# Kernel optimization log

Hardware: AMD Instinct MI355X
Metric: run time of the kernel (lower is better)

## Reference

```python
import jax, jax.numpy as jnp
import numpy as np

B, N, C, H = 8, 2048, 384, 6
D = C // H  # head dim = 64
SCALE = D ** -0.5


def setup_inputs() -> dict:
    key = jax.random.key(0)
    k1, k2, k3, k4 = jax.random.split(key, 4)
    x = jax.random.normal(k1, (B, N, C), dtype=jnp.float32)
    prompt = jnp.zeros((1,), dtype=jnp.float32)  # unused by forward
    mask = jax.random.uniform(k2, (B, N, N), dtype=jnp.float32)
    qkv_w = jax.random.normal(k3, (3 * C, C), dtype=jnp.float32) * (C ** -0.5)
    proj_w = jax.random.normal(k4, (C, C), dtype=jnp.float32) * (C ** -0.5)
    proj_b = jnp.zeros((C,), dtype=jnp.float32)
    return {"x": x, "prompt": prompt, "mask": mask,
            "qkv_w": qkv_w, "proj_w": proj_w, "proj_b": proj_b}


def reference(x, prompt, mask, qkv_w, proj_w, proj_b):
    b, n, c = x.shape
    # qkv: Linear(dim, 3*dim, bias=False) -> (B,N,3,H,D) -> (3,B,H,N,D)
    qkv = (x @ qkv_w.T).reshape(b, n, 3, H, D).transpose(2, 0, 3, 1, 4)
    q, k, v = qkv[0], qkv[1], qkv[2]
    # attn scores with additive mask (mask * -1e5), softmax over keys
    attn = jnp.einsum('bhqd,bhkd->bhqk', q, k) * SCALE
    attn = attn + (mask * -100000.0)[:, None, :, :]
    attn = jax.nn.softmax(attn, axis=-1)
    out = jnp.einsum('bhqk,bhkd->bhqd', attn, v)  # (B,H,N,D)
    out = out.transpose(0, 2, 1, 3).reshape(b, n, c)
    return out @ proj_w.T + proj_b
```

## Files before the change

kernel.cpp:

```cpp
#include <hip/hip_runtime.h>
#include <stdint.h>
#include <math.h>

#define BB 8
#define SEQ 2048
#define CDIM 384
#define NH 6
#define HD 64
#define QKVN 1152

typedef __attribute__((ext_vector_type(8))) __bf16 bf16x8;
typedef __attribute__((ext_vector_type(4))) __bf16 bf16x4;
typedef __attribute__((ext_vector_type(4))) float f32x4;
typedef __attribute__((ext_vector_type(4))) unsigned short ushort4v;

__device__ __forceinline__ unsigned short f2bf(float f) {
  unsigned int u = __float_as_uint(f);
  u += 0x7fffu + ((u >> 16) & 1u);
  return (unsigned short)(u >> 16);
}

__global__ void k_convert(const float* __restrict__ src, unsigned short* __restrict__ dst, int n4) {
  int i = blockIdx.x * blockDim.x + threadIdx.x;
  if (i >= n4) return;
  float4 f = reinterpret_cast<const float4*>(src)[i];
  ushort4v u;
  u.x = f2bf(f.x); u.y = f2bf(f.y); u.z = f2bf(f.z); u.w = f2bf(f.w);
  reinterpret_cast<ushort4v*>(dst)[i] = u;
}

__device__ __forceinline__ void gload_lds16(const unsigned short* g, unsigned short* l) {
  __builtin_amdgcn_global_load_lds((const __attribute__((address_space(1))) void*)g,
                                   (__attribute__((address_space(3))) void*)l, 16, 0, 0);
}

template<int OUT_F32>
__global__ __launch_bounds__(256, 2) void k_gemm_bt(
    const unsigned short* __restrict__ A, const unsigned short* __restrict__ Bm,
    unsigned short* __restrict__ Cb, float* __restrict__ Cf,
    const float* __restrict__ bias, int M, int Nc, int K)
{
  __shared__ unsigned short lA[128 * 32];
  __shared__ unsigned short lB[128 * 32];
  const int t = threadIdx.x;
  const int w = t >> 6, l = t & 63;
  const int wr = w >> 1, wc = w & 1;
  const int row0 = blockIdx.x * 128, col0 = blockIdx.y * 128;
  const f32x4 vzero = {0.f, 0.f, 0.f, 0.f};
  f32x4 acc[4][4];
#pragma unroll
  for (int m = 0; m < 4; ++m)
#pragma unroll
    for (int n = 0; n < 4; ++n) acc[m][n] = vzero;

  const int srow = w * 16 + (l >> 2);
  const int scol = (l & 3) * 8;
  const int lr = l & 15, kc = (l >> 4) * 8;

  for (int k0 = 0; k0 < K; k0 += 32) {
#pragma unroll
    for (int r = 0; r < 2; ++r) {
      gload_lds16(A + (size_t)(row0 + r * 64 + srow) * K + k0 + scol,
                  &lA[(r * 64 + srow) * 32 + scol]);
      gload_lds16(Bm + (size_t)(col0 + r * 64 + srow) * K + k0 + scol,
                  &lB[(r * 64 + srow) * 32 + scol]);
    }
    __syncthreads();
    bf16x8 af[4], bfr[4];
#pragma unroll
    for (int m = 0; m < 4; ++m)
      af[m] = *(const bf16x8*)&lA[(wr * 64 + m * 16 + lr) * 32 + kc];
#pragma unroll
    for (int n = 0; n < 4; ++n)
      bfr[n] = *(const bf16x8*)&lB[(wc * 64 + n * 16 + lr) * 32 + kc];
#pragma unroll
    for (int m = 0; m < 4; ++m)
#pragma unroll
      for (int n = 0; n < 4; ++n)
        acc[m][n] = __builtin_amdgcn_mfma_f32_16x16x32_bf16(af[m], bfr[n], acc[m][n], 0, 0, 0);
    __syncthreads();
  }

#pragma unroll
  for (int m = 0; m < 4; ++m) {
    const int row = row0 + wr * 64 + m * 16 + (l >> 4) * 4;
#pragma unroll
    for (int n = 0; n < 4; ++n) {
      const int col = col0 + wc * 64 + n * 16 + (l & 15);
      if (OUT_F32) {
        const float bv = bias[col];
#pragma unroll
        for (int j = 0; j < 4; ++j)
          Cf[(size_t)(row + j) * Nc + col] = acc[m][n][j] + bv;
      } else {
#pragma unroll
        for (int j = 0; j < 4; ++j)
          Cb[(size_t)(row + j) * Nc + col] = f2bf(acc[m][n][j]);
      }
    }
  }
}

__global__ void k_vtrans(const unsigned short* __restrict__ qkv, unsigned short* __restrict__ vt)
{
  __shared__ unsigned short tile[64][76];
  const int bh = blockIdx.x;
  const int b = bh / NH, h = bh - b * NH;
  const int n0 = blockIdx.y * 64;
  const int t = threadIdx.x;
  const int rr0 = t >> 4;
  const int c4 = (t & 15) * 4;
  const unsigned short* src = qkv + (size_t)(b * SEQ + n0) * QKVN + 2 * CDIM + h * HD;
#pragma unroll
  for (int rr = 0; rr < 4; ++rr) {
    int n = rr * 16 + rr0;
    ushort4v v = *(const ushort4v*)(src + (size_t)n * QKVN + c4);
    *(ushort4v*)&tile[n][c4] = v;
  }
  __syncthreads();
  unsigned short* dst = vt + (size_t)bh * HD * SEQ + n0;
#pragma unroll
  for (int rr = 0; rr < 4; ++rr) {
    int d = rr * 16 + rr0;
    ushort4v v;
    v.x = tile[c4 + 0][d];
    v.y = tile[c4 + 1][d];
    v.z = tile[c4 + 2][d];
    v.w = tile[c4 + 3][d];
    *(ushort4v*)(dst + (size_t)d * SEQ + c4) = v;
  }
}

__global__ __launch_bounds__(256, 3) void k_attn(
    const unsigned short* __restrict__ qkv, const float* __restrict__ mask,
    const unsigned short* __restrict__ vt, unsigned short* __restrict__ aout)
{
  const int bid = blockIdx.x;
  const int b = bid & 7;
  const int g2 = bid >> 3;
  const int h = g2 % NH;
  const int nt = g2 / NH;
  const int t = threadIdx.x;
  const int w = t >> 6, l = t & 63;
  const int gk = l >> 4, c = l & 15;
  const int q0 = nt * 128 + w * 16;

  __shared__ unsigned short lK[2][4096];
  __shared__ unsigned short lV[2][4096];

  const unsigned short* qb0 = qkv + (size_t)(b * SEQ + q0) * QKVN + h * HD;
  const unsigned short* qb1 = qb0 + (size_t)64 * QKVN;
  const unsigned short* kb = qkv + (size_t)(b * SEQ) * QKVN + CDIM + h * HD;
  const unsigned short* vb = vt + (size_t)(b * NH + h) * HD * SEQ;
  const float* mrow0 = mask + ((size_t)b * SEQ + q0 + c) * SEQ + 4 * gk;
  const float* mrow1 = mrow0 + (size_t)64 * SEQ;

  const int trow = t >> 3, tg = t & 7;
  const int glog = tg ^ (trow & 7);
  const size_t kSrc = (size_t)trow * QKVN + glog * 8;
  const size_t vSrc = (size_t)trow * SEQ + glog * 8;
  const int tid8 = t * 8;

  const int fr0 = c * 64 + ((gk) ^ (c & 7)) * 8;
  const int fr1 = c * 64 + ((4 + gk) ^ (c & 7)) * 8;
  const int cx2 = 2 * (c & 7);
  const int vg0 = c * 64 + ((gk) ^ cx2) * 4;
  const int vg1 = c * 64 + ((4 + gk) ^ cx2) * 4;
  const int vg2 = c * 64 + ((8 + gk) ^ cx2) * 4;
  const int vg3 = c * 64 + ((12 + gk) ^ cx2) * 4;

  bf16x8 qf00 = *(const bf16x8*)(qb0 + (size_t)c * QKVN + gk * 8);
  bf16x8 qf01 = *(const bf16x8*)(qb0 + (size_t)c * QKVN + 32 + gk * 8);
  bf16x8 qf10 = *(const bf16x8*)(qb1 + (size_t)c * QKVN + gk * 8);
  bf16x8 qf11 = *(const bf16x8*)(qb1 + (size_t)c * QKVN + 32 + gk * 8);
#pragma unroll
  for (int i = 0; i < 8; ++i) {
    qf00[i] = (__bf16)((float)qf00[i] * 0.18033688f);
    qf01[i] = (__bf16)((float)qf01[i] * 0.18033688f);
    qf10[i] = (__bf16)((float)qf10[i] * 0.18033688f);
    qf11[i] = (__bf16)((float)qf11[i] * 0.18033688f);
  }

  const __bf16 one = (__bf16)1.0f;
  const bf16x8 vones = {one, one, one, one, one, one, one, one};
  const f32x4 vzero = {0.f, 0.f, 0.f, 0.f};
  f32x4 acco0[4], acco1[4];
  f32x4 asum0 = vzero, asum1 = vzero;
  float mreg0 = -INFINITY, mreg1 = -INFINITY;
#pragma unroll
  for (int dt = 0; dt < 4; ++dt) { acco0[dt] = vzero; acco1[dt] = vzero; }

#pragma unroll
  for (int j = 0; j < 2; ++j) {
    gload_lds16(kb + (size_t)j * 32 * QKVN + kSrc, &lK[0][j * 2048 + tid8]);
    gload_lds16(vb + (size_t)j * 32 * SEQ + vSrc, &lV[0][j * 2048 + tid8]);
  }
  int buf = 0;

  for (int kt = 0; kt < SEQ; kt += 64) {
    const bool haveNext = (kt + 64 < SEQ);
    __syncthreads();
    if (haveNext) {
#pragma unroll
      for (int j = 0; j < 2; ++j) {
        gload_lds16(kb + (size_t)(kt + 64 + j * 32) * QKVN + kSrc, &lK[buf ^ 1][j * 2048 + tid8]);
        gload_lds16(vb + (kt + 64) + (size_t)j * 32 * SEQ + vSrc, &lV[buf ^ 1][j * 2048 + tid8]);
      }
    }

    float4 mk0[4], mk1[4];
#pragma unroll
    for (int j = 0; j < 4; ++j) {
      mk0[j] = *(const float4*)(mrow0 + kt + 16 * j);
      mk1[j] = *(const float4*)(mrow1 + kt + 16 * j);
    }

    f32x4 s0[4], s1[4];
    __builtin_amdgcn_s_setprio(1);
#pragma unroll
    for (int j = 0; j < 4; ++j) {
      bf16x8 kfa = *(const bf16x8*)&lK[buf][j * 1024 + fr0];
      bf16x8 kfb = *(const bf16x8*)&lK[buf][j * 1024 + fr1];
      s0[j] = __builtin_amdgcn_mfma_f32_16x16x32_bf16(kfa, qf00, vzero, 0, 0, 0);
      s0[j] = __builtin_amdgcn_mfma_f32_16x16x32_bf16(kfb, qf01, s0[j], 0, 0, 0);
      s1[j] = __builtin_amdgcn_mfma_f32_16x16x32_bf16(kfa, qf10, vzero, 0, 0, 0);
      s1[j] = __builtin_amdgcn_mfma_f32_16x16x32_bf16(kfb, qf11, s1[j], 0, 0, 0);
    }
    __builtin_amdgcn_s_setprio(0);

#pragma unroll
    for (int j = 0; j < 4; ++j) {
      const float* m0 = (const float*)&mk0[j];
      const float* m1 = (const float*)&mk1[j];
#pragma unroll
      for (int r = 0; r < 4; ++r) {
        s0[j][r] = fmaf(m0[r], -144269.50f, s0[j][r]);
        s1[j][r] = fmaf(m1[r], -144269.50f, s1[j][r]);
      }
    }

    float a0 = fmaxf(fmaxf(s0[0][0], s0[0][1]), s0[0][2]);
    float b0 = fmaxf(fmaxf(s0[0][3], s0[1][0]), s0[1][1]);
    float d0 = fmaxf(fmaxf(s0[1][2], s0[1][3]), s0[2][0]);
    float e0 = fmaxf(fmaxf(s0[2][1], s0[2][2]), s0[2][3]);
    float f0 = fmaxf(fmaxf(s0[3][0], s0[3][1]), s0[3][2]);
    float tm0 = fmaxf(fmaxf(fmaxf(a0, b0), d0), fmaxf(fmaxf(e0, f0), s0[3][3]));
    float a1 = fmaxf(fmaxf(s1[0][0], s1[0][1]), s1[0][2]);
    float b1 = fmaxf(fmaxf(s1[0][3], s1[1][0]), s1[1][1]);
    float d1 = fmaxf(fmaxf(s1[1][2], s1[1][3]), s1[2][0]);
    float e1 = fmaxf(fmaxf(s1[2][1], s1[2][2]), s1[2][3]);
    float f1 = fmaxf(fmaxf(s1[3][0], s1[3][1]), s1[3][2]);
    float tm1 = fmaxf(fmaxf(fmaxf(a1, b1), d1), fmaxf(fmaxf(e1, f1), s1[3][3]));
    tm0 = fmaxf(tm0, __shfl_xor(tm0, 16));
    tm1 = fmaxf(tm1, __shfl_xor(tm1, 16));
    tm0 = fmaxf(tm0, __shfl_xor(tm0, 32));
    tm1 = fmaxf(tm1, __shfl_xor(tm1, 32));

    if (__any(tm0 > mreg0 + 8.f)) {
      const float mn = fmaxf(mreg0, tm0);
      const float al = __builtin_amdgcn_exp2f(mreg0 - mn);
      mreg0 = mn;
      float alr[4];
#pragma unroll
      for (int r = 0; r < 4; ++r) alr[r] = __shfl(al, 20 * gk + r);
#pragma unroll
      for (int r = 0; r < 4; ++r) asum0[r] *= alr[r];
#pragma unroll
      for (int dt = 0; dt < 4; ++dt)
#pragma unroll
        for (int r = 0; r < 4; ++r) acco0[dt][r] *= alr[r];
    }
    if (__any(tm1 > mreg1 + 8.f)) {
      const float mn = fmaxf(mreg1, tm1);
      const float al = __builtin_amdgcn_exp2f(mreg1 - mn);
      mreg1 = mn;
      float alr[4];
#pragma unroll
      for (int r = 0; r < 4; ++r) alr[r] = __shfl(al, 20 * gk + r);
#pragma unroll
      for (int r = 0; r < 4; ++r) asum1[r] *= alr[r];
#pragma unroll
      for (int dt = 0; dt < 4; ++dt)
#pragma unroll
        for (int r = 0; r < 4; ++r) acco1[dt][r] *= alr[r];
    }

#pragma unroll
    for (int j = 0; j < 4; ++j)
#pragma unroll
      for (int r = 0; r < 4; ++r) {
        s0[j][r] = __builtin_amdgcn_exp2f(s0[j][r] - mreg0);
        s1[j][r] = __builtin_amdgcn_exp2f(s1[j][r] - mreg1);
      }

    union { unsigned int u[8]; bf16x8 v[2]; } pu0, pu1;
#pragma unroll
    for (int j = 0; j < 4; ++j) {
      asm("v_cvt_pk_bf16_f32 %0, %1, %2" : "=v"(pu0.u[2 * j]) : "v"(s0[j][0]), "v"(s0[j][1]));
      asm("v_cvt_pk_bf16_f32 %0, %1, %2" : "=v"(pu0.u[2 * j + 1]) : "v"(s0[j][2]), "v"(s0[j][3]));
      asm("v_cvt_pk_bf16_f32 %0, %1, %2" : "=v"(pu1.u[2 * j]) : "v"(s1[j][0]), "v"(s1[j][1]));
      asm("v_cvt_pk_bf16_f32 %0, %1, %2" : "=v"(pu1.u[2 * j + 1]) : "v"(s1[j][2]), "v"(s1[j][3]));
    }

    __builtin_amdgcn_s_setprio(1);
    asum0 = __builtin_amdgcn_mfma_f32_16x16x32_bf16(pu0.v[0], vones, asum0, 0, 0, 0);
    asum0 = __builtin_amdgcn_mfma_f32_16x16x32_bf16(pu0.v[1], vones, asum0, 0, 0, 0);
    asum1 = __builtin_amdgcn_mfma_f32_16x16x32_bf16(pu1.v[0], vones, asum1, 0, 0, 0);
    asum1 = __builtin_amdgcn_mfma_f32_16x16x32_bf16(pu1.v[1], vones, asum1, 0, 0, 0);
#pragma unroll
    for (int dt = 0; dt < 4; ++dt) {
      const unsigned short* vrow = &lV[buf][dt * 1024];
      bf16x4 a0v = *(const bf16x4*)(vrow + vg0);
      bf16x4 a1v = *(const bf16x4*)(vrow + vg1);
      bf16x4 a2v = *(const bf16x4*)(vrow + vg2);
      bf16x4 a3v = *(const bf16x4*)(vrow + vg3);
      bf16x8 vf0 = __builtin_shufflevector(a0v, a1v, 0, 1, 2, 3, 4, 5, 6, 7);
      bf16x8 vf1 = __builtin_shufflevector(a2v, a3v, 0, 1, 2, 3, 4, 5, 6, 7);
      acco0[dt] = __builtin_amdgcn_mfma_f32_16x16x32_bf16(pu0.v[0], vf0, acco0[dt], 0, 0, 0);
      acco0[dt] = __builtin_amdgcn_mfma_f32_16x16x32_bf16(pu0.v[1], vf1, acco0[dt], 0, 0, 0);
      acco1[dt] = __builtin_amdgcn_mfma_f32_16x16x32_bf16(pu1.v[0], vf0, acco1[dt], 0, 0, 0);
      acco1[dt] = __builtin_amdgcn_mfma_f32_16x16x32_bf16(pu1.v[1], vf1, acco1[dt], 0, 0, 0);
    }
    __builtin_amdgcn_s_setprio(0);
    buf ^= 1;
  }

  float inv0[4], inv1[4];
#pragma unroll
  for (int r = 0; r < 4; ++r) {
    inv0[r] = 1.0f / asum0[r];
    inv1[r] = 1.0f / asum1[r];
  }
  unsigned short* ob0 = aout + (size_t)(b * SEQ + q0) * CDIM + h * HD;
  unsigned short* ob1 = ob0 + (size_t)64 * CDIM;
#pragma unroll
  for (int r = 0; r < 4; ++r)
#pragma unroll
    for (int dt = 0; dt < 4; ++dt) {
      ob0[(size_t)(4 * gk + r) * CDIM + dt * 16 + c] = f2bf(acco0[dt][r] * inv0[r]);
      ob1[(size_t)(4 * gk + r) * CDIM + dt * 16 + c] = f2bf(acco1[dt][r] * inv1[r]);
    }
}

extern "C" void kernel_launch(void* const* d_in, const int* in_sizes, int n_in,
                              void* d_out, int out_size, void* d_ws, size_t ws_size,
                              hipStream_t stream) {
  (void)in_sizes; (void)n_in; (void)out_size; (void)ws_size;
  const float* x      = (const float*)d_in[0];
  const float* mask   = (const float*)d_in[2];
  const float* qkv_w  = (const float*)d_in[3];
  const float* proj_w = (const float*)d_in[4];
  const float* proj_b = (const float*)d_in[5];
  float* out = (float*)d_out;
  char* ws = (char*)d_ws;

  unsigned short* xb    = (unsigned short*)(ws + 0);
  unsigned short* wqb   = (unsigned short*)(ws + 12582912);
  unsigned short* wpb   = (unsigned short*)(ws + 13467648);
  unsigned short* qkvb  = (unsigned short*)(ws + 13762560);
  unsigned short* vtb   = (unsigned short*)(ws + 51511296);
  unsigned short* aoutb = (unsigned short*)(ws + 64094208);

  k_convert<<<6144, 256, 0, stream>>>(x, xb, 1572864);
  k_convert<<<432, 256, 0, stream>>>(qkv_w, wqb, 110592);
  k_convert<<<144, 256, 0, stream>>>(proj_w, wpb, 36864);
  k_gemm_bt<0><<<dim3(128, 9), 256, 0, stream>>>(xb, wqb, qkvb, nullptr, nullptr, 16384, 1152, 384);
  k_vtrans<<<dim3(48, 32), 256, 0, stream>>>(qkvb, vtb);
  k_attn<<<768, 256, 0, stream>>>(qkvb, mask, vtb, aoutb);
  k_gemm_bt<1><<<dim3(128, 3), 256, 0, stream>>>(aoutb, wpb, nullptr, out, proj_b, 16384, 384, 384);
}
```

Measured before the change: 174.4 us.

## Software-pipeline PV MFMA of previous tile with QK of current tile

Restructures the attention loop so the P·V and row-sum MFMAs for the previous key tile run right after the QK MFMAs of the current tile, before that tile's softmax. The V tile ring becomes a triple buffer so the previous tile's V stays resident while the next one is loaded. A final PV step after the loop handles the last tile. The aim is to overlap the matrix-core work with the exp/max VALU work, at the cost of more LDS and more registers, since the packed P values stay live across iterations.

```diff
diff --git a/kernel.cpp b/kernel.cpp
--- a/kernel.cpp
+++ b/kernel.cpp
@@ -146,7 +146,7 @@
   const int q0 = nt * 128 + w * 16;
 
   __shared__ unsigned short lK[2][4096];
-  __shared__ unsigned short lV[2][4096];
+  __shared__ unsigned short lV[3][4096];
 
   const unsigned short* qb0 = qkv + (size_t)(b * SEQ + q0) * QKVN + h * HD;
   const unsigned short* qb1 = qb0 + (size_t)64 * QKVN;
@@ -190,12 +190,17 @@
 #pragma unroll
   for (int dt = 0; dt < 4; ++dt) { acco0[dt] = vzero; acco1[dt] = vzero; }
 
+  union PU { unsigned int u[8]; bf16x8 v[2]; };
+  PU pu0 = {}, pu1 = {};
+
 #pragma unroll
   for (int j = 0; j < 2; ++j) {
     gload_lds16(kb + (size_t)j * 32 * QKVN + kSrc, &lK[0][j * 2048 + tid8]);
     gload_lds16(vb + (size_t)j * 32 * SEQ + vSrc, &lV[0][j * 2048 + tid8]);
   }
-  int buf = 0;
+  int bufK = 0;
+  int vst = 1;
+  int vpv = 2;
 
   for (int kt = 0; kt < SEQ; kt += 64) {
     const bool haveNext = (kt + 64 < SEQ);
@@ -203,8 +208,8 @@
     if (haveNext) {
 #pragma unroll
       for (int j = 0; j < 2; ++j) {
-        gload_lds16(kb + (size_t)(kt + 64 + j * 32) * QKVN + kSrc, &lK[buf ^ 1][j * 2048 + tid8]);
-        gload_lds16(vb + (kt + 64) + (size_t)j * 32 * SEQ + vSrc, &lV[buf ^ 1][j * 2048 + tid8]);
+        gload_lds16(kb + (size_t)(kt + 64 + j * 32) * QKVN + kSrc, &lK[bufK ^ 1][j * 2048 + tid8]);
+        gload_lds16(vb + (kt + 64) + (size_t)j * 32 * SEQ + vSrc, &lV[vst][j * 2048 + tid8]);
       }
     }
 
@@ -219,12 +224,32 @@
     __builtin_amdgcn_s_setprio(1);
 #pragma unroll
     for (int j = 0; j < 4; ++j) {
-      bf16x8 kfa = *(const bf16x8*)&lK[buf][j * 1024 + fr0];
-      bf16x8 kfb = *(const bf16x8*)&lK[buf][j * 1024 + fr1];
+      bf16x8 kfa = *(const bf16x8*)&lK[bufK][j * 1024 + fr0];
+      bf16x8 kfb = *(const bf16x8*)&lK[bufK][j * 1024 + fr1];
       s0[j] = __builtin_amdgcn_mfma_f32_16x16x32_bf16(kfa, qf00, vzero, 0, 0, 0);
       s0[j] = __builtin_amdgcn_mfma_f32_16x16x32_bf16(kfb, qf01, s0[j], 0, 0, 0);
       s1[j] = __builtin_amdgcn_mfma_f32_16x16x32_bf16(kfa, qf10, vzero, 0, 0, 0);
       s1[j] = __builtin_amdgcn_mfma_f32_16x16x32_bf16(kfb, qf11, s1[j], 0, 0, 0);
+    }
+    if (kt > 0) {
+      asum0 = __builtin_amdgcn_mfma_f32_16x16x32_bf16(pu0.v[0], vones, asum0, 0, 0, 0);
+      asum0 = __builtin_amdgcn_mfma_f32_16x16x32_bf16(pu0.v[1], vones, asum0, 0, 0, 0);
+      asum1 = __builtin_amdgcn_mfma_f32_16x16x32_bf16(pu1.v[0], vones, asum1, 0, 0, 0);
+      asum1 = __builtin_amdgcn_mfma_f32_16x16x32_bf16(pu1.v[1], vones, asum1, 0, 0, 0);
+#pragma unroll
+      for (int dt = 0; dt < 4; ++dt) {
+        const unsigned short* vrow = &lV[vpv][dt * 1024];
+        bf16x4 a0v = *(const bf16x4*)(vrow + vg0);
+        bf16x4 a1v = *(const bf16x4*)(vrow + vg1);
+        bf16x4 a2v = *(const bf16x4*)(vrow + vg2);
+        bf16x4 a3v = *(const bf16x4*)(vrow + vg3);
+        bf16x8 vf0 = __builtin_shufflevector(a0v, a1v, 0, 1, 2, 3, 4, 5, 6, 7);
+        bf16x8 vf1 = __builtin_shufflevector(a2v, a3v, 0, 1, 2, 3, 4, 5, 6, 7);
+        acco0[dt] = __builtin_amdgcn_mfma_f32_16x16x32_bf16(pu0.v[0], vf0, acco0[dt], 0, 0, 0);
+        acco0[dt] = __builtin_amdgcn_mfma_f32_16x16x32_bf16(pu0.v[1], vf1, acco0[dt], 0, 0, 0);
+        acco1[dt] = __builtin_amdgcn_mfma_f32_16x16x32_bf16(pu1.v[0], vf0, acco1[dt], 0, 0, 0);
+        acco1[dt] = __builtin_amdgcn_mfma_f32_16x16x32_bf16(pu1.v[1], vf1, acco1[dt], 0, 0, 0);
+      }
     }
     __builtin_amdgcn_s_setprio(0);
 
@@ -292,8 +317,6 @@
         s0[j][r] = __builtin_amdgcn_exp2f(s0[j][r] - mreg0);
         s1[j][r] = __builtin_amdgcn_exp2f(s1[j][r] - mreg1);
       }
-
-    union { unsigned int u[8]; bf16x8 v[2]; } pu0, pu1;
 #pragma unroll
     for (int j = 0; j < 4; ++j) {
       asm("v_cvt_pk_bf16_f32 %0, %1, %2" : "=v"(pu0.u[2 * j]) : "v"(s0[j][0]), "v"(s0[j][1]));
@@ -302,27 +325,28 @@
       asm("v_cvt_pk_bf16_f32 %0, %1, %2" : "=v"(pu1.u[2 * j + 1]) : "v"(s1[j][2]), "v"(s1[j][3]));
     }
 
-    __builtin_amdgcn_s_setprio(1);
-    asum0 = __builtin_amdgcn_mfma_f32_16x16x32_bf16(pu0.v[0], vones, asum0, 0, 0, 0);
-    asum0 = __builtin_amdgcn_mfma_f32_16x16x32_bf16(pu0.v[1], vones, asum0, 0, 0, 0);
-    asum1 = __builtin_amdgcn_mfma_f32_16x16x32_bf16(pu1.v[0], vones, asum1, 0, 0, 0);
-    asum1 = __builtin_amdgcn_mfma_f32_16x16x32_bf16(pu1.v[1], vones, asum1, 0, 0, 0);
-#pragma unroll
-    for (int dt = 0; dt < 4; ++dt) {
-      const unsigned short* vrow = &lV[buf][dt * 1024];
-      bf16x4 a0v = *(const bf16x4*)(vrow + vg0);
-      bf16x4 a1v = *(const bf16x4*)(vrow + vg1);
-      bf16x4 a2v = *(const bf16x4*)(vrow + vg2);
-      bf16x4 a3v = *(const bf16x4*)(vrow + vg3);
-      bf16x8 vf0 = __builtin_shufflevector(a0v, a1v, 0, 1, 2, 3, 4, 5, 6, 7);
-      bf16x8 vf1 = __builtin_shufflevector(a2v, a3v, 0, 1, 2, 3, 4, 5, 6, 7);
-      acco0[dt] = __builtin_amdgcn_mfma_f32_16x16x32_bf16(pu0.v[0], vf0, acco0[dt], 0, 0, 0);
-      acco0[dt] = __builtin_amdgcn_mfma_f32_16x16x32_bf16(pu0.v[1], vf1, acco0[dt], 0, 0, 0);
-      acco1[dt] = __builtin_amdgcn_mfma_f32_16x16x32_bf16(pu1.v[0], vf0, acco1[dt], 0, 0, 0);
-      acco1[dt] = __builtin_amdgcn_mfma_f32_16x16x32_bf16(pu1.v[1], vf1, acco1[dt], 0, 0, 0);
-    }
-    __builtin_amdgcn_s_setprio(0);
-    buf ^= 1;
+    bufK ^= 1;
+    vst = (vst == 2) ? 0 : vst + 1;
+    vpv = (vpv == 2) ? 0 : vpv + 1;
+  }
+
+  asum0 = __builtin_amdgcn_mfma_f32_16x16x32_bf16(pu0.v[0], vones, asum0, 0, 0, 0);
+  asum0 = __builtin_amdgcn_mfma_f32_16x16x32_bf16(pu0.v[1], vones, asum0, 0, 0, 0);
+  asum1 = __builtin_amdgcn_mfma_f32_16x16x32_bf16(pu1.v[0], vones, asum1, 0, 0, 0);
+  asum1 = __builtin_amdgcn_mfma_f32_16x16x32_bf16(pu1.v[1], vones, asum1, 0, 0, 0);
+#pragma unroll
+  for (int dt = 0; dt < 4; ++dt) {
+    const unsigned short* vrow = &lV[vpv][dt * 1024];
+    bf16x4 a0v = *(const bf16x4*)(vrow + vg0);
+    bf16x4 a1v = *(const bf16x4*)(vrow + vg1);
+    bf16x4 a2v = *(const bf16x4*)(vrow + vg2);
+    bf16x4 a3v = *(const bf16x4*)(vrow + vg3);
+    bf16x8 vf0 = __builtin_shufflevector(a0v, a1v, 0, 1, 2, 3, 4, 5, 6, 7);
+    bf16x8 vf1 = __builtin_shufflevector(a2v, a3v, 0, 1, 2, 3, 4, 5, 6, 7);
+    acco0[dt] = __builtin_amdgcn_mfma_f32_16x16x32_bf16(pu0.v[0], vf0, acco0[dt], 0, 0, 0);
+    acco0[dt] = __builtin_amdgcn_mfma_f32_16x16x32_bf16(pu0.v[1], vf1, acco0[dt], 0, 0, 0);
+    acco1[dt] = __builtin_amdgcn_mfma_f32_16x16x32_bf16(pu1.v[0], vf0, acco1[dt], 0, 0, 0);
+    acco1[dt] = __builtin_amdgcn_mfma_f32_16x16x32_bf16(pu1.v[1], vf1, acco1[dt], 0, 0, 0);
   }
 
   float inv0[4], inv1[4];
```

New measurement: 257.1 us. 47.4% more time.
